# Kernel optimization log

Measured on AMD Instinct MI355X. Metric: run time of the kernel, lower is better.

Reference implementation:

```python
import jax, jax.numpy as jnp
import numpy as np

NQ = 14
DIM = 2 ** NQ


def make_unitary(M):
    # QR-based unitarization, matching torch: Q * (diag(R)/|diag(R)|) broadcast over rows
    Q, R = jnp.linalg.qr(M)
    d = jnp.diagonal(R, axis1=-2, axis2=-1)
    ph = d / jnp.abs(d)
    return Q * ph[..., None, :]


def apply_1q(state, U, q, nq):
    # state: [B] + [2]*nq, qubit q lives at axis 1 + (nq-1-q) (qubit 0 = LSB)
    ax = 1 + (nq - 1 - q)
    s = jnp.moveaxis(state, ax, 1)
    shp = s.shape
    s = s.reshape(shp[0], 2, -1)
    s = jnp.einsum('ji,bir->bjr', U, s)
    return jnp.moveaxis(s.reshape(shp), 1, ax)


def apply_1q_batched(state, U, q, nq):
    # U: [B,2,2] per-batch gate
    ax = 1 + (nq - 1 - q)
    s = jnp.moveaxis(state, ax, 1)
    shp = s.shape
    s = s.reshape(shp[0], 2, -1)
    s = jnp.einsum('bji,bir->bjr', U, s)
    return jnp.moveaxis(s.reshape(shp), 1, ax)


def apply_2q(state, U4, qa, qb, nq):
    # source: gate index = bit_qa + 2*bit_qb, so reshape(4,4)->(2,2,2,2) gives [ob,oa,ib,ia]
    G = U4.reshape(2, 2, 2, 2)
    ax_a = 1 + (nq - 1 - qa)
    ax_b = 1 + (nq - 1 - qb)
    s = jnp.moveaxis(state, (ax_b, ax_a), (1, 2))
    shp = s.shape
    s = s.reshape(shp[0], 2, 2, -1)
    s = jnp.einsum('JKjk,bjkr->bJKr', G, s)
    return jnp.moveaxis(s.reshape(shp), (1, 2), (ax_b, ax_a))


def setup_inputs() -> dict:
    key = jax.random.key(0)
    ks = jax.random.split(key, 9)
    B, H = 256, 1024
    return {
        'x': jax.random.normal(ks[0], (B, H), dtype=jnp.float32),
        'w_pre': jax.random.normal(ks[1], (2 * NQ, H), dtype=jnp.float32) * 0.03,
        'b_pre': jax.random.normal(ks[2], (2 * NQ,), dtype=jnp.float32) * 0.01,
        'w_post': jax.random.normal(ks[3], (H, DIM), dtype=jnp.float32) * 0.01,
        'b_post': jax.random.normal(ks[4], (H,), dtype=jnp.float32) * 0.01,
        'sq_re': jax.random.normal(ks[5], (NQ, 2, 2), dtype=jnp.float32),
        'sq_im': jax.random.normal(ks[6], (NQ, 2, 2), dtype=jnp.float32),
        'ent_re': jax.random.normal(ks[7], (NQ - 1, 4, 4), dtype=jnp.float32),
        'ent_im': jax.random.normal(ks[8], (NQ - 1, 4, 4), dtype=jnp.float32),
    }


def reference(x, w_pre, b_pre, w_post, b_post, sq_re, sq_im, ent_re, ent_im):
    B = x.shape[0]
    nq = NQ
    # pre_quantum Linear
    params = x @ w_pre.T + b_pre  # [B, 2*nq]
    theta = params[:, 0::2]
    phi = params[:, 1::2]
    c = jnp.cos(theta / 2)
    s = jnp.sin(theta / 2)
    # initial state = rotation gates applied to |0...0>: keep only column 0 of each gate
    v = jnp.stack([c.astype(jnp.complex64), (jnp.exp(1j * phi) * s).astype(jnp.complex64)], axis=-1)  # [B,nq,2]
    state = v[:, nq - 1]  # MSB axis first (qubit nq-1)
    for q in range(nq - 2, -1, -1):
        state = (state[:, :, None] * v[:, q][:, None, :]).reshape(B, -1)
    state = state.reshape((B,) + (2,) * nq)
    # learned unitaries (batched QR over gate index)
    sq = make_unitary(sq_re.astype(jnp.complex64) + 1j * sq_im.astype(jnp.complex64))
    ent = make_unitary(ent_re.astype(jnp.complex64) + 1j * ent_im.astype(jnp.complex64))
    for q in range(nq):
        state = apply_1q(state, sq[q], q, nq)
    for q in range(nq - 1):
        state = apply_2q(state, ent[q], q, q + 1, nq)
    amp = state.reshape(B, -1)  # C-order flatten => index = sum(bit_q << q), matches source
    probs = amp.real ** 2 + amp.imag ** 2  # [B, dim]
    return probs @ w_post.T + b_post  # [B, hidden]
```

## Files before the change

### kernel.cpp

```cpp
#include <hip/hip_runtime.h>
#include <hip/hip_bf16.h>
#include <math.h>

#define NQ 14
#define DIM 16384
#define NB 256
#define NH 1024
#define SPLITK 16
#define KCHUNK (DIM / SPLITK)
#define BK 64

typedef __attribute__((ext_vector_type(8))) short bf16x8;
typedef __attribute__((ext_vector_type(4))) float f32x4;

#define SW(i) ((i) + 5 * ((i) >> 5))
#define SW_SIZE (DIM + 5 * (DIM / 32))

template <int N>
__device__ void gs_qr(const float* Mre, const float* Mim, float* Uout) {
    double qre[N][N], qim[N][N];
#pragma unroll
    for (int j = 0; j < N; j++) {
        double vr[N], vi[N];
#pragma unroll
        for (int r = 0; r < N; r++) { vr[r] = (double)Mre[r * N + j]; vi[r] = (double)Mim[r * N + j]; }
#pragma unroll
        for (int i = 0; i < N; i++) {
            if (i < j) {
                double rr = 0.0, ri = 0.0;
#pragma unroll
                for (int r = 0; r < N; r++) {
                    rr += qre[i][r] * vr[r] + qim[i][r] * vi[r];
                    ri += qre[i][r] * vi[r] - qim[i][r] * vr[r];
                }
#pragma unroll
                for (int r = 0; r < N; r++) {
                    vr[r] -= rr * qre[i][r] - ri * qim[i][r];
                    vi[r] -= rr * qim[i][r] + ri * qre[i][r];
                }
            }
        }
        double nn = 0.0;
#pragma unroll
        for (int r = 0; r < N; r++) nn += vr[r] * vr[r] + vi[r] * vi[r];
        double inv = 1.0 / sqrt(nn);
#pragma unroll
        for (int r = 0; r < N; r++) { qre[j][r] = vr[r] * inv; qim[j][r] = vi[r] * inv; }
    }
#pragma unroll
    for (int r = 0; r < N; r++)
#pragma unroll
        for (int j = 0; j < N; j++) {
            Uout[(r * N + j) * 2]     = (float)qre[j][r];
            Uout[(r * N + j) * 2 + 1] = (float)qim[j][r];
        }
}

__global__ __launch_bounds__(256) void k_pre(const float* __restrict__ x,
                                             const float* __restrict__ w_pre,
                                             const float* __restrict__ b_pre,
                                             const float* __restrict__ sq_re,
                                             const float* __restrict__ sq_im,
                                             const float* __restrict__ ent_re,
                                             const float* __restrict__ ent_im,
                                             float* __restrict__ v_buf,
                                             float* __restrict__ sqU,
                                             float* __restrict__ entU) {
    const int b = blockIdx.x;
    const int t = threadIdx.x;
    if (b >= NB) {
        if (b == NB) {
            if (t < NQ) gs_qr<2>(sq_re + t * 4, sq_im + t * 4, sqU + t * 8);
        } else {
            if (t < NQ - 1) gs_qr<4>(ent_re + t * 16, ent_im + t * 16, entU + t * 32);
        }
        return;
    }
    __shared__ float red[28][4];

    float4 xs = ((const float4*)(x + (size_t)b * NH))[t];
    float acc[28];
#pragma unroll
    for (int j = 0; j < 28; j++) {
        float4 w = ((const float4*)(w_pre + (size_t)j * NH))[t];
        acc[j] = xs.x * w.x + xs.y * w.y + xs.z * w.z + xs.w * w.w;
    }
    int lane = t & 63, wv = t >> 6;
#pragma unroll
    for (int j = 0; j < 28; j++) {
        float a = acc[j];
#pragma unroll
        for (int o = 32; o > 0; o >>= 1) a += __shfl_down(a, o);
        if (lane == 0) red[j][wv] = a;
    }
    __syncthreads();
    if (t < NQ) {
        float p0 = red[2*t][0] + red[2*t][1] + red[2*t][2] + red[2*t][3] + b_pre[2*t];
        float p1 = red[2*t+1][0] + red[2*t+1][1] + red[2*t+1][2] + red[2*t+1][3] + b_pre[2*t+1];
        float c = cosf(p0 * 0.5f), s = sinf(p0 * 0.5f);
        float cp = cosf(p1), sp = sinf(p1);
        ((float4*)v_buf)[b * NQ + t] = make_float4(c, 0.f, cp * s, sp * s);
    }
}

#define APPLY_GATE(I, GP) do {                                                \
    _Pragma("unroll")                                                         \
    for (int g_ = 0; g_ < 4; g_++) {                                          \
        const int base_ = (I)==0 ? (g_<<2) : ((I)==1 ? ((g_&1)|((g_>>1)<<3)) : g_); \
        float xr_[4], xi_[4];                                                 \
        _Pragma("unroll")                                                     \
        for (int c_ = 0; c_ < 4; c_++) { xr_[c_] = ar[base_+(c_<<(I))]; xi_[c_] = ai[base_+(c_<<(I))]; } \
        _Pragma("unroll")                                                     \
        for (int r_ = 0; r_ < 4; r_++) {                                      \
            float nr_ = 0.f, ni_ = 0.f;                                       \
            _Pragma("unroll")                                                 \
            for (int c_ = 0; c_ < 4; c_++) {                                  \
                const float grc_ = (GP)[(r_*4+c_)*2];                         \
                const float gic_ = (GP)[(r_*4+c_)*2+1];                       \
                nr_ += grc_*xr_[c_] - gic_*xi_[c_];                           \
                ni_ += grc_*xi_[c_] + gic_*xr_[c_];                           \
            }                                                                 \
            ar[base_+(r_<<(I))] = nr_; ai[base_+(r_<<(I))] = ni_;             \
        }                                                                     \
    }                                                                         \
} while (0)

#define IDX_W0(r) (((t) << 4) | (r))
#define IDX_W1(r) (((t) & 7) | ((r) << 3) | (((t) >> 3) << 7))
#define IDX_W2(r) (((t) & 63) | ((r) << 6) | (((t) >> 6) << 10))
#define IDX_W3(r) (((t) & 511) | ((r) << 9) | (((t) >> 9) << 13))
#define IDX_W4(r) ((t) | ((r) << 10))

#define TRANSPOSE(IDX_OLD, IDX_NEW) do {                                      \
    _Pragma("unroll")                                                         \
    for (int r_ = 0; r_ < 16; r_++) {                                         \
        int o_ = SW(IDX_OLD(r_));                                             \
        sre[o_] = ar[r_]; simg[o_] = ai[r_];                                  \
    }                                                                         \
    __syncthreads();                                                          \
    _Pragma("unroll")                                                         \
    for (int r_ = 0; r_ < 16; r_++) {                                         \
        int n_ = SW(IDX_NEW(r_));                                             \
        ar[r_] = sre[n_]; ai[r_] = simg[n_];                                  \
    }                                                                         \
} while (0)

extern __shared__ float smem[];
__global__ __launch_bounds__(1024) void k_state(const float* __restrict__ v_buf,
                                                const float* __restrict__ sqU,
                                                const float* __restrict__ entU,
                                                __hip_bfloat16* __restrict__ probs) {
    const int b = blockIdx.x, t = threadIdx.x;
    float* sre  = smem;
    float* simg = smem + SW_SIZE;
    float* wloc = smem + 2 * SW_SIZE;

    if (t < NQ) {
        float4 v = ((const float4*)v_buf)[b * NQ + t];
        const float* u = sqU + t * 8;
        float w0r = u[0]*v.x - u[1]*v.y + u[2]*v.z - u[3]*v.w;
        float w0i = u[0]*v.y + u[1]*v.x + u[2]*v.w + u[3]*v.z;
        float w1r = u[4]*v.x - u[5]*v.y + u[6]*v.z - u[7]*v.w;
        float w1i = u[4]*v.y + u[5]*v.x + u[6]*v.w + u[7]*v.z;
        wloc[t*4+0] = w0r; wloc[t*4+1] = w0i; wloc[t*4+2] = w1r; wloc[t*4+3] = w1i;
    }
    __syncthreads();

    float ar[16], ai[16];
    {
        float cr = 1.f, ci = 0.f;
#pragma unroll
        for (int q = 4; q < 14; q++) {
            int bit = (t >> (q - 4)) & 1;
            float br = wloc[q*4 + 2*bit], bi = wloc[q*4 + 2*bit + 1];
            float nr = cr*br - ci*bi, ni = cr*bi + ci*br;
            cr = nr; ci = ni;
        }
        float p01r[4], p01i[4], p23r[4], p23i[4];
#pragma unroll
        for (int j = 0; j < 4; j++) {
            int b0 = j & 1, b1 = j >> 1;
            float a0r = wloc[0*4 + 2*b0], a0i = wloc[0*4 + 2*b0 + 1];
            float a1r = wloc[1*4 + 2*b1], a1i = wloc[1*4 + 2*b1 + 1];
            p01r[j] = a0r*a1r - a0i*a1i; p01i[j] = a0r*a1i + a0i*a1r;
            float a2r = wloc[2*4 + 2*b0], a2i = wloc[2*4 + 2*b0 + 1];
            float a3r = wloc[3*4 + 2*b1], a3i = wloc[3*4 + 2*b1 + 1];
            p23r[j] = a2r*a3r - a2i*a3i; p23i[j] = a2r*a3i + a2i*a3r;
        }
#pragma unroll
        for (int r = 0; r < 16; r++) {
            int lo = r & 3, hi2 = r >> 2;
            float tr = cr*p01r[lo] - ci*p01i[lo];
            float ti = cr*p01i[lo] + ci*p01r[lo];
            ar[r] = tr*p23r[hi2] - ti*p23i[hi2];
            ai[r] = tr*p23i[hi2] + ti*p23r[hi2];
        }
    }

    APPLY_GATE(0, entU + 0*32);
    APPLY_GATE(1, entU + 1*32);
    APPLY_GATE(2, entU + 2*32);
    TRANSPOSE(IDX_W0, IDX_W1);
    APPLY_GATE(0, entU + 3*32);
    APPLY_GATE(1, entU + 4*32);
    APPLY_GATE(2, entU + 5*32);
    __syncthreads();
    TRANSPOSE(IDX_W1, IDX_W2);
    APPLY_GATE(0, entU + 6*32);
    APPLY_GATE(1, entU + 7*32);
    APPLY_GATE(2, entU + 8*32);
    __syncthreads();
    TRANSPOSE(IDX_W2, IDX_W3);
    APPLY_GATE(0, entU + 9*32);
    APPLY_GATE(1, entU + 10*32);
    APPLY_GATE(2, entU + 11*32);
    __syncthreads();
    TRANSPOSE(IDX_W3, IDX_W4);
    APPLY_GATE(2, entU + 12*32);

#pragma unroll
    for (int r = 0; r < 16; r++) {
        float pr = ar[r]*ar[r] + ai[r]*ai[r];
        probs[(size_t)b * DIM + (r << 10) + t] = __float2bfloat16(pr);
    }
}

__global__ __launch_bounds__(512) void k_gemm_mfma(const ushort* __restrict__ A,
                                                   const float* __restrict__ Bw,
                                                   float* __restrict__ part) {
    __shared__ ushort As[128 * 64];
    __shared__ ushort Bs[128 * 64];
    const int t = threadIdx.x;
    const int l = t & 63, wid = t >> 6;
    const int wr = wid >> 2, wc = wid & 3;
    const int bm0 = blockIdx.x * 128;
    const int hn0 = blockIdx.y * 128;
    const int k0  = blockIdx.z * KCHUNK;

    f32x4 acc[4][2];
#pragma unroll
    for (int m = 0; m < 4; m++)
#pragma unroll
        for (int n = 0; n < 2; n++) acc[m][n] = (f32x4){0.f, 0.f, 0.f, 0.f};

    const int srow = t >> 3;
    const int scol = (t & 7) * 8;
    const int alr  = l >> 3;
    const int alc  = (l & 7) * 8;

    for (int kc = 0; kc < KCHUNK; kc += BK) {
        const int kbase = k0 + kc;
#pragma unroll
        for (int i = 0; i < 2; i++) {
            const int r0 = i * 64 + wid * 8;
            const ushort* gsrc = A + (size_t)(bm0 + r0 + alr) * DIM + kbase + alc;
            __builtin_amdgcn_global_load_lds(
                (const __attribute__((address_space(1))) unsigned int*)gsrc,
                (__attribute__((address_space(3))) unsigned int*)&As[r0 * 64],
                16, 0, 0);
        }
#pragma unroll
        for (int i = 0; i < 2; i++) {
            const int r = i * 64 + srow;
            const float* bsrc = Bw + (size_t)(hn0 + r) * DIM + kbase + scol;
            float4 b0 = *(const float4*)(bsrc);
            float4 b1 = *(const float4*)(bsrc + 4);
            union { ushort u[8]; bf16x8 v; } pk;
            __hip_bfloat16 h;
            h = __float2bfloat16(b0.x); pk.u[0] = *(ushort*)&h;
            h = __float2bfloat16(b0.y); pk.u[1] = *(ushort*)&h;
            h = __float2bfloat16(b0.z); pk.u[2] = *(ushort*)&h;
            h = __float2bfloat16(b0.w); pk.u[3] = *(ushort*)&h;
            h = __float2bfloat16(b1.x); pk.u[4] = *(ushort*)&h;
            h = __float2bfloat16(b1.y); pk.u[5] = *(ushort*)&h;
            h = __float2bfloat16(b1.z); pk.u[6] = *(ushort*)&h;
            h = __float2bfloat16(b1.w); pk.u[7] = *(ushort*)&h;
            *(bf16x8*)&Bs[r * 64 + scol] = pk.v;
        }
        __syncthreads();
#pragma unroll
        for (int kk = 0; kk < 2; kk++) {
            const int kcol = kk * 32 + (l >> 4) * 8;
            bf16x8 a[4], b[2];
#pragma unroll
            for (int m = 0; m < 4; m++)
                a[m] = *(const bf16x8*)&As[(wr * 64 + m * 16 + (l & 15)) * 64 + kcol];
#pragma unroll
            for (int n = 0; n < 2; n++)
                b[n] = *(const bf16x8*)&Bs[(wc * 32 + n * 16 + (l & 15)) * 64 + kcol];
#pragma unroll
            for (int m = 0; m < 4; m++)
#pragma unroll
                for (int n = 0; n < 2; n++)
                    acc[m][n] = __builtin_amdgcn_mfma_f32_16x16x32_bf16(
                        a[m], b[n], acc[m][n], 0, 0, 0);
        }
        __syncthreads();
    }
    float* dst = part + (size_t)blockIdx.z * (NB * NH);
#pragma unroll
    for (int m = 0; m < 4; m++) {
        const int row = bm0 + wr * 64 + m * 16 + (l >> 4) * 4;
#pragma unroll
        for (int n = 0; n < 2; n++) {
            const int col = hn0 + wc * 32 + n * 16 + (l & 15);
#pragma unroll
            for (int j = 0; j < 4; j++)
                dst[(size_t)(row + j) * NH + col] = acc[m][n][j];
        }
    }
}

__global__ __launch_bounds__(256) void k_reduce(const float* __restrict__ part,
                                                const float* __restrict__ b_post,
                                                float* __restrict__ out) {
    int i = blockIdx.x * 256 + threadIdx.x;
    float s = b_post[i & (NH - 1)];
#pragma unroll
    for (int z = 0; z < SPLITK; z++) s += part[(size_t)z * (NB * NH) + i];
    out[i] = s;
}

extern "C" void kernel_launch(void* const* d_in, const int* in_sizes, int n_in,
                              void* d_out, int out_size, void* d_ws, size_t ws_size,
                              hipStream_t stream) {
    const float* x      = (const float*)d_in[0];
    const float* w_pre  = (const float*)d_in[1];
    const float* b_pre  = (const float*)d_in[2];
    const float* w_post = (const float*)d_in[3];
    const float* b_post = (const float*)d_in[4];
    const float* sq_re  = (const float*)d_in[5];
    const float* sq_im  = (const float*)d_in[6];
    const float* ent_re = (const float*)d_in[7];
    const float* ent_im = (const float*)d_in[8];
    float* out = (float*)d_out;
    char* ws   = (char*)d_ws;

    float* v_buf          = (float*)(ws);
    float* sqU            = (float*)(ws + 57344);
    float* entU           = (float*)(ws + 57792);
    __hip_bfloat16* probs = (__hip_bfloat16*)(ws + 59456);
    float* part           = (float*)(ws + 8448064);

    k_pre<<<NB + 2, 256, 0, stream>>>(x, w_pre, b_pre, sq_re, sq_im, ent_re, ent_im,
                                      v_buf, sqU, entU);

    const int smem_bytes = (2 * SW_SIZE + NQ * 4) * 4;
    (void)hipFuncSetAttribute((const void*)k_state,
                              hipFuncAttributeMaxDynamicSharedMemorySize, smem_bytes);
    k_state<<<NB, 1024, smem_bytes, stream>>>(v_buf, sqU, entU, probs);

    k_gemm_mfma<<<dim3(2, 8, SPLITK), 512, 0, stream>>>((const ushort*)probs, w_post, part);
    k_reduce<<<(NB * NH) / 256, 256, 0, stream>>>(part, b_post, out);
}
```

Before: 192.9 us.

## Double-buffer GEMM LDS tiles and halve M tile to double grid size

The post-GEMM kernel now double-buffers its A and B shared-memory tiles: it prefetches the next K slice (async global-to-LDS for A, register loads for the fp32 weights) while MFMAs run on the current buffer, leaving one barrier per iteration. The M tile shrinks from 128 to 64, so the grid grows from 256 to 512 blocks for better CU occupancy. In exchange, the w_post fp32 weights are read and converted twice as often across blocks, and register pressure rises from the prefetched values.

```diff
diff --git a/kernel.cpp b/kernel.cpp
--- a/kernel.cpp
+++ b/kernel.cpp
@@ -9,6 +9,8 @@
 #define SPLITK 16
 #define KCHUNK (DIM / SPLITK)
 #define BK 64
+#define BM 64
+#define BN 128
 
 typedef __attribute__((ext_vector_type(8))) short bf16x8;
 typedef __attribute__((ext_vector_type(4))) float f32x4;
@@ -228,79 +230,104 @@
 __global__ __launch_bounds__(512) void k_gemm_mfma(const ushort* __restrict__ A,
                                                    const float* __restrict__ Bw,
                                                    float* __restrict__ part) {
-    __shared__ ushort As[128 * 64];
-    __shared__ ushort Bs[128 * 64];
+    __shared__ ushort As[2][BM * BK];
+    __shared__ ushort Bs[2][BN * BK];
     const int t = threadIdx.x;
     const int l = t & 63, wid = t >> 6;
     const int wr = wid >> 2, wc = wid & 3;
-    const int bm0 = blockIdx.x * 128;
-    const int hn0 = blockIdx.y * 128;
+    const int bm0 = blockIdx.x * BM;
+    const int hn0 = blockIdx.y * BN;
     const int k0  = blockIdx.z * KCHUNK;
 
-    f32x4 acc[4][2];
-#pragma unroll
-    for (int m = 0; m < 4; m++)
+    f32x4 acc[2][2];
+#pragma unroll
+    for (int m = 0; m < 2; m++)
 #pragma unroll
         for (int n = 0; n < 2; n++) acc[m][n] = (f32x4){0.f, 0.f, 0.f, 0.f};
 
-    const int srow = t >> 3;
-    const int scol = (t & 7) * 8;
-    const int alr  = l >> 3;
-    const int alc  = (l & 7) * 8;
-
+    const int brow = t >> 3;
+    const int bcol = (t & 7) * 8;
+
+#define ISSUE_A(BUF, KB)                                                      \
+    __builtin_amdgcn_global_load_lds(                                         \
+        (const __attribute__((address_space(1))) unsigned int*)               \
+            (A + (size_t)(bm0 + wid * 8 + (l >> 3)) * DIM + (KB) + (l & 7) * 8), \
+        (__attribute__((address_space(3))) unsigned int*)&As[BUF][wid * 8 * BK], \
+        16, 0, 0)
+
+#define PACK_B(BUF, I, V0, V1) do {                                           \
+    union { ushort u[8]; bf16x8 v; } pk_;                                     \
+    __hip_bfloat16 h_;                                                        \
+    h_ = __float2bfloat16((V0).x); pk_.u[0] = *(ushort*)&h_;                  \
+    h_ = __float2bfloat16((V0).y); pk_.u[1] = *(ushort*)&h_;                  \
+    h_ = __float2bfloat16((V0).z); pk_.u[2] = *(ushort*)&h_;                  \
+    h_ = __float2bfloat16((V0).w); pk_.u[3] = *(ushort*)&h_;                  \
+    h_ = __float2bfloat16((V1).x); pk_.u[4] = *(ushort*)&h_;                  \
+    h_ = __float2bfloat16((V1).y); pk_.u[5] = *(ushort*)&h_;                  \
+    h_ = __float2bfloat16((V1).z); pk_.u[6] = *(ushort*)&h_;                  \
+    h_ = __float2bfloat16((V1).w); pk_.u[7] = *(ushort*)&h_;                  \
+    *(bf16x8*)&Bs[BUF][((I) * 64 + brow) * BK + bcol] = pk_.v;                \
+} while (0)
+
+    {
+        float4 p0[2], p1[2];
+#pragma unroll
+        for (int i = 0; i < 2; i++) {
+            const float* src = Bw + (size_t)(hn0 + i * 64 + brow) * DIM + k0 + bcol;
+            p0[i] = ((const float4*)src)[0];
+            p1[i] = ((const float4*)src)[1];
+        }
+        ISSUE_A(0, k0);
+#pragma unroll
+        for (int i = 0; i < 2; i++) PACK_B(0, i, p0[i], p1[i]);
+        __syncthreads();
+    }
+
+    int cur = 0;
     for (int kc = 0; kc < KCHUNK; kc += BK) {
-        const int kbase = k0 + kc;
-#pragma unroll
-        for (int i = 0; i < 2; i++) {
-            const int r0 = i * 64 + wid * 8;
-            const ushort* gsrc = A + (size_t)(bm0 + r0 + alr) * DIM + kbase + alc;
-            __builtin_amdgcn_global_load_lds(
-                (const __attribute__((address_space(1))) unsigned int*)gsrc,
-                (__attribute__((address_space(3))) unsigned int*)&As[r0 * 64],
-                16, 0, 0);
-        }
-#pragma unroll
-        for (int i = 0; i < 2; i++) {
-            const int r = i * 64 + srow;
-            const float* bsrc = Bw + (size_t)(hn0 + r) * DIM + kbase + scol;
-            float4 b0 = *(const float4*)(bsrc);
-            float4 b1 = *(const float4*)(bsrc + 4);
-            union { ushort u[8]; bf16x8 v; } pk;
-            __hip_bfloat16 h;
-            h = __float2bfloat16(b0.x); pk.u[0] = *(ushort*)&h;
-            h = __float2bfloat16(b0.y); pk.u[1] = *(ushort*)&h;
-            h = __float2bfloat16(b0.z); pk.u[2] = *(ushort*)&h;
-            h = __float2bfloat16(b0.w); pk.u[3] = *(ushort*)&h;
-            h = __float2bfloat16(b1.x); pk.u[4] = *(ushort*)&h;
-            h = __float2bfloat16(b1.y); pk.u[5] = *(ushort*)&h;
-            h = __float2bfloat16(b1.z); pk.u[6] = *(ushort*)&h;
-            h = __float2bfloat16(b1.w); pk.u[7] = *(ushort*)&h;
-            *(bf16x8*)&Bs[r * 64 + scol] = pk.v;
-        }
-        __syncthreads();
+        const bool has_next = (kc + BK) < KCHUNK;
+        float4 nb0[2], nb1[2];
+        if (has_next) {
+            const int kb = k0 + kc + BK;
+#pragma unroll
+            for (int i = 0; i < 2; i++) {
+                const float* src = Bw + (size_t)(hn0 + i * 64 + brow) * DIM + kb + bcol;
+                nb0[i] = ((const float4*)src)[0];
+                nb1[i] = ((const float4*)src)[1];
+            }
+            ISSUE_A(cur ^ 1, kb);
+        }
 #pragma unroll
         for (int kk = 0; kk < 2; kk++) {
             const int kcol = kk * 32 + (l >> 4) * 8;
-            bf16x8 a[4], b[2];
-#pragma unroll
-            for (int m = 0; m < 4; m++)
-                a[m] = *(const bf16x8*)&As[(wr * 64 + m * 16 + (l & 15)) * 64 + kcol];
+            bf16x8 a[2], b[2];
+#pragma unroll
+            for (int m = 0; m < 2; m++)
+                a[m] = *(const bf16x8*)&As[cur][(wr * 32 + m * 16 + (l & 15)) * BK + kcol];
 #pragma unroll
             for (int n = 0; n < 2; n++)
-                b[n] = *(const bf16x8*)&Bs[(wc * 32 + n * 16 + (l & 15)) * 64 + kcol];
-#pragma unroll
-            for (int m = 0; m < 4; m++)
+                b[n] = *(const bf16x8*)&Bs[cur][(wc * 32 + n * 16 + (l & 15)) * BK + kcol];
+#pragma unroll
+            for (int m = 0; m < 2; m++)
 #pragma unroll
                 for (int n = 0; n < 2; n++)
                     acc[m][n] = __builtin_amdgcn_mfma_f32_16x16x32_bf16(
                         a[m], b[n], acc[m][n], 0, 0, 0);
         }
+        if (has_next) {
+#pragma unroll
+            for (int i = 0; i < 2; i++) PACK_B(cur ^ 1, i, nb0[i], nb1[i]);
+        }
         __syncthreads();
-    }
+        cur ^= 1;
+    }
+#undef ISSUE_A
+#undef PACK_B
+
     float* dst = part + (size_t)blockIdx.z * (NB * NH);
 #pragma unroll
-    for (int m = 0; m < 4; m++) {
-        const int row = bm0 + wr * 64 + m * 16 + (l >> 4) * 4;
+    for (int m = 0; m < 2; m++) {
+        const int row = bm0 + wr * 32 + m * 16 + (l >> 4) * 4;
 #pragma unroll
         for (int n = 0; n < 2; n++) {
             const int col = hn0 + wc * 32 + n * 16 + (l & 15);
@@ -350,6 +377,6 @@
                               hipFuncAttributeMaxDynamicSharedMemorySize, smem_bytes);
     k_state<<<NB, 1024, smem_bytes, stream>>>(v_buf, sqU, entU, probs);
 
-    k_gemm_mfma<<<dim3(2, 8, SPLITK), 512, 0, stream>>>((const ushort*)probs, w_post, part);
+    k_gemm_mfma<<<dim3(NB / BM, NH / BN, SPLITK), 512, 0, stream>>>((const ushort*)probs, w_post, part);
     k_reduce<<<(NB * NH) / 256, 256, 0, stream>>>(part, b_post, out);
 }
```

New measurement: 198.2 us. 2.8% more time.
